# Kernel tuning notes

Measured on AMD Instinct MI355X. Metric: run time of the kernel, lower is better.

## Reference

```python
import jax, jax.numpy as jnp
import numpy as np

DIM = 256      # z feature dim
HEADS = 8
C = 64         # per-head dim == x channel dim
INNER = HEADS * C  # 512


def setup_inputs() -> dict:
    key = jax.random.key(0)
    ks = jax.random.split(key, 8)
    b, h, w, m = 8, 64, 64, 256
    x = jax.random.normal(ks[0], (b, C, h, w), dtype=jnp.float32)
    z = jax.random.normal(ks[1], (b, m, DIM), dtype=jnp.float32)
    s = 1.0 / np.sqrt(DIM)
    Wk = jax.random.normal(ks[2], (DIM, INNER), dtype=jnp.float32) * s
    bk = jnp.zeros((INNER,), dtype=jnp.float32)
    Wv = jax.random.normal(ks[3], (DIM, INNER), dtype=jnp.float32) * s
    bv = jnp.zeros((INNER,), dtype=jnp.float32)
    Wo = jax.random.normal(ks[4], (INNER, C), dtype=jnp.float32) * (1.0 / np.sqrt(INNER))
    bo = jnp.zeros((C,), dtype=jnp.float32)
    return {"x": x, "z": z, "Wk": Wk, "bk": bk, "Wv": Wv, "bv": bv, "Wo": Wo, "bo": bo}


def reference(x, z, Wk, bk, Wv, bv, Wo, bo):
    b, c, h, w = x.shape
    m = z.shape[1]
    heads = Wk.shape[1] // c
    hw = h * w
    # Faithful to torch: raw view (b,c,h,w)->(b,hw,c), then repeat along feature
    # dim and raw view into (b, heads, hw, c).
    q = jnp.tile(x.reshape(b, hw, c), (1, 1, heads)).reshape(b, heads, hw, c)
    # k/v: Linear then raw view (b, m, heads*c) -> (b, heads, m, c).
    k = (z @ Wk + bk).reshape(b, heads, m, c)
    v = (z @ Wv + bv).reshape(b, heads, m, c)
    scale = c ** (-0.5)
    dots = jnp.einsum('bhlc,bhmc->bhlm', q, k) * scale
    attn = jax.nn.softmax(dots, axis=-1)
    out = jnp.einsum('bhlm,bhmc->bhlc', attn, v)
    out = jnp.transpose(out, (0, 2, 1, 3)).reshape(b, hw, heads * c)  # b l (h c)
    out = out @ Wo + bo  # (b, hw, c)
    # Faithful raw view back to (b, c, h, w), then residual.
    return x + out.reshape(b, c, h, w)
```

## Files before the change

### kernel.cpp

```cpp
#include <hip/hip_runtime.h>

#define HEADS 8
#define CH    64
#define HW    4096
#define MTOK  256
#define DIMZ  256
#define INNER 512
#define LROWS 512

typedef __attribute__((ext_vector_type(8))) __bf16 bf16x8;
typedef __attribute__((ext_vector_type(4))) float  f32x4;

__device__ __forceinline__ unsigned f2bf(float f) {
  unsigned u = __float_as_uint(f);
  return (u + 0x7fffu + ((u >> 16) & 1u)) >> 16;
}

__device__ __forceinline__ bf16x8 ld_bf8(const unsigned short* p) {
  uint4 v = *(const uint4*)p;
  return __builtin_bit_cast(bf16x8, v);
}

__global__ __launch_bounds__(256) void prep(
    const float* __restrict__ z, const float* __restrict__ Wk,
    const float* __restrict__ Wv, const float* __restrict__ Wo,
    unsigned short* __restrict__ zbf, unsigned short* __restrict__ WkT,
    unsigned short* __restrict__ WvT, unsigned short* __restrict__ WoT) {
  const int blk = blockIdx.x, tid = threadIdx.x;
  if (blk < 512) {
    int i = (blk * 256 + tid) * 4;
    float4 f = *(const float4*)(z + i);
    uint2 w;
    w.x = f2bf(f.x) | (f2bf(f.y) << 16);
    w.y = f2bf(f.z) | (f2bf(f.w) << 16);
    *(uint2*)(zbf + i) = w;
  } else if (blk < 768) {
    const bool isK = blk < 640;
    const float* __restrict__ W = isK ? Wk : Wv;
    unsigned short* __restrict__ WT = isK ? WkT : WvT;
    int gidx = (blk - (isK ? 512 : 640)) * 256 + tid;
    int n = gidx >> 6, k0 = (gidx & 63) * 4;
    uint2 w;
    w.x = f2bf(W[(size_t)k0 * INNER + n])       | (f2bf(W[(size_t)(k0 + 1) * INNER + n]) << 16);
    w.y = f2bf(W[(size_t)(k0 + 2) * INNER + n]) | (f2bf(W[(size_t)(k0 + 3) * INNER + n]) << 16);
    *(uint2*)(WT + (size_t)n * DIMZ + k0) = w;
  } else {
    int gidx = (blk - 768) * 256 + tid;
    int n = gidx >> 7, k0 = (gidx & 127) * 4;
    uint2 w;
    w.x = f2bf(Wo[(size_t)k0 * CH + n])       | (f2bf(Wo[(size_t)(k0 + 1) * CH + n]) << 16);
    w.y = f2bf(Wo[(size_t)(k0 + 2) * CH + n]) | (f2bf(Wo[(size_t)(k0 + 3) * CH + n]) << 16);
    *(uint2*)(WoT + (size_t)n * INNER + k0) = w;
  }
}

__global__ __launch_bounds__(256) void kv_mfma(
    const unsigned short* __restrict__ zbf,
    const unsigned short* __restrict__ WkT, const float* __restrict__ bk,
    const unsigned short* __restrict__ WvT, const float* __restrict__ bv,
    unsigned short* __restrict__ klin, unsigned short* __restrict__ vt) {
  const int t = threadIdx.x;
  const int lane = t & 63, wid = t >> 6;
  const int c = lane & 15, g = lane >> 4;
  const int mb = blockIdx.x;
  const int bn = blockIdx.y;
  const bool isK = bn < 8;
  const int nb = bn & 7;
  const unsigned short* __restrict__ WT = isK ? WkT : WvT;
  const float* __restrict__ bias = isK ? bk : bv;
  const int m0 = mb * 64 + (wid >> 1) * 32;
  const int n0 = nb * 64 + (wid & 1) * 32;

  f32x4 acc[2][2];
#pragma unroll
  for (int i = 0; i < 2; ++i)
#pragma unroll
    for (int j = 0; j < 2; ++j) acc[i][j] = (f32x4)0.f;

#pragma unroll
  for (int s = 0; s < 8; ++s) {
    const int k0 = s * 32;
    bf16x8 a0 = ld_bf8(zbf + (size_t)(m0 + c) * DIMZ + k0 + 8 * g);
    bf16x8 a1 = ld_bf8(zbf + (size_t)(m0 + 16 + c) * DIMZ + k0 + 8 * g);
    bf16x8 b0 = ld_bf8(WT + (size_t)(n0 + c) * DIMZ + k0 + 8 * g);
    bf16x8 b1 = ld_bf8(WT + (size_t)(n0 + 16 + c) * DIMZ + k0 + 8 * g);
    if (isK) {
      acc[0][0] = __builtin_amdgcn_mfma_f32_16x16x32_bf16(b0, a0, acc[0][0], 0, 0, 0);
      acc[0][1] = __builtin_amdgcn_mfma_f32_16x16x32_bf16(b1, a0, acc[0][1], 0, 0, 0);
      acc[1][0] = __builtin_amdgcn_mfma_f32_16x16x32_bf16(b0, a1, acc[1][0], 0, 0, 0);
      acc[1][1] = __builtin_amdgcn_mfma_f32_16x16x32_bf16(b1, a1, acc[1][1], 0, 0, 0);
    } else {
      acc[0][0] = __builtin_amdgcn_mfma_f32_16x16x32_bf16(a0, b0, acc[0][0], 0, 0, 0);
      acc[0][1] = __builtin_amdgcn_mfma_f32_16x16x32_bf16(a0, b1, acc[0][1], 0, 0, 0);
      acc[1][0] = __builtin_amdgcn_mfma_f32_16x16x32_bf16(a1, b0, acc[1][0], 0, 0, 0);
      acc[1][1] = __builtin_amdgcn_mfma_f32_16x16x32_bf16(a1, b1, acc[1][1], 0, 0, 0);
    }
  }

  if (isK) {
#pragma unroll
    for (int mt = 0; mt < 2; ++mt)
#pragma unroll
      for (int nt = 0; nt < 2; ++nt) {
        const int m = m0 + mt * 16 + c;
        const int n = n0 + nt * 16 + 4 * g;
        float4 b4 = *(const float4*)(bias + n);
        uint2 w;
        w.x = f2bf(acc[mt][nt][0] + b4.x) | (f2bf(acc[mt][nt][1] + b4.y) << 16);
        w.y = f2bf(acc[mt][nt][2] + b4.z) | (f2bf(acc[mt][nt][3] + b4.w) << 16);
        *(uint2*)(klin + (size_t)m * INNER + n) = w;
      }
  } else {
#pragma unroll
    for (int mt = 0; mt < 2; ++mt)
#pragma unroll
      for (int nt = 0; nt < 2; ++nt) {
        const int n = n0 + nt * 16 + c;
        const float bn1 = bias[n];
        const int m = m0 + mt * 16 + 4 * g;
        const int bb = m >> 8;
        const int mtk = m & 255;
        const int h = mtk >> 5, t0 = mtk & 31;
        const int cc = n & 63, cb = n >> 6;
        uint2 w;
        w.x = f2bf(acc[mt][nt][0] + bn1) | (f2bf(acc[mt][nt][1] + bn1) << 16);
        w.y = f2bf(acc[mt][nt][2] + bn1) | (f2bf(acc[mt][nt][3] + bn1) << 16);
        *(uint2*)(vt + ((size_t)((bb * HEADS + h) * CH + cc)) * MTOK + cb * 32 + t0) = w;
      }
  }
}

__global__ __launch_bounds__(64) void attn_mfma(
    const float* __restrict__ x,
    const unsigned short* __restrict__ kbf,
    const unsigned short* __restrict__ vtbf,
    unsigned short* __restrict__ out2) {
  __shared__ unsigned short Psh[16 * 256];
  char* Pb = (char*)Psh;
  const int t = threadIdx.x;
  const int c = t & 15, g = t >> 4;
  const int bid = blockIdx.x;
  const int lt = bid & 31, hh = (bid >> 5) & 7, b = bid >> 8;
  const int qbase = lt * 16;
  const float* xs = x + (size_t)b * (HW * CH) + (size_t)hh * (LROWS * CH);
  const unsigned short* Kg = kbf + ((size_t)b * MTOK + hh * 32) * INNER;
  const unsigned short* Vg = vtbf + (size_t)(b * HEADS + hh) * (CH * MTOK);

  const float qs = 0.125f * 1.44269504089f;
  bf16x8 qfr[2];
#pragma unroll
  for (int ks = 0; ks < 2; ++ks) {
    const float* qp = xs + (size_t)(qbase + c) * CH + 32 * ks + 8 * g;
    float4 f0 = *(const float4*)qp;
    float4 f1 = *(const float4*)(qp + 4);
    uint4 u;
    u.x = f2bf(f0.x * qs) | (f2bf(f0.y * qs) << 16);
    u.y = f2bf(f0.z * qs) | (f2bf(f0.w * qs) << 16);
    u.z = f2bf(f1.x * qs) | (f2bf(f1.y * qs) << 16);
    u.w = f2bf(f1.z * qs) | (f2bf(f1.w * qs) << 16);
    qfr[ks] = __builtin_bit_cast(bf16x8, u);
  }

  f32x4 acc[16];
#pragma unroll
  for (int kf = 0; kf < 16; ++kf) acc[kf] = (f32x4)0.f;
#pragma unroll
  for (int kf = 0; kf < 16; ++kf) {
    const unsigned short* kp =
        Kg + (size_t)((kf & 1) * 16 + c) * INNER + (kf >> 1) * 64 + 8 * g;
    bf16x8 a0 = ld_bf8(kp);
    bf16x8 a1 = ld_bf8(kp + 32);
    acc[kf] = __builtin_amdgcn_mfma_f32_16x16x32_bf16(a0, qfr[0], acc[kf], 0, 0, 0);
    acc[kf] = __builtin_amdgcn_mfma_f32_16x16x32_bf16(a1, qfr[1], acc[kf], 0, 0, 0);
  }

  float m = acc[0][0];
#pragma unroll
  for (int kf = 0; kf < 16; ++kf)
    m = fmaxf(m, fmaxf(fmaxf(acc[kf][0], acc[kf][1]),
                       fmaxf(acc[kf][2], acc[kf][3])));
  m = fmaxf(m, __shfl_xor(m, 16));
  m = fmaxf(m, __shfl_xor(m, 32));
  float sum = 0.f;
  const int rowb = c * 512;
#pragma unroll
  for (int kf = 0; kf < 16; ++kf) {
    float e0 = exp2f(acc[kf][0] - m);
    float e1 = exp2f(acc[kf][1] - m);
    float e2 = exp2f(acc[kf][2] - m);
    float e3 = exp2f(acc[kf][3] - m);
    sum += (e0 + e1) + (e2 + e3);
    uint2 w;
    w.x = f2bf(e0) | (f2bf(e1) << 16);
    w.y = f2bf(e2) | (f2bf(e3) << 16);
    int off = (rowb + (16 * kf + 4 * g) * 2) ^ ((c & 7) << 4);
    *(uint2*)(Pb + off) = w;
  }
  sum += __shfl_xor(sum, 16);
  sum += __shfl_xor(sum, 32);
  const float inv = 1.f / sum;
  asm volatile("" ::: "memory");

  f32x4 o[4];
#pragma unroll
  for (int cf = 0; cf < 4; ++cf) o[cf] = (f32x4)0.f;
#pragma unroll
  for (int ks = 0; ks < 8; ++ks) {
    bf16x8 p = __builtin_bit_cast(bf16x8,
        *(const uint4*)(Pb + ((c * 512 + (32 * ks + 8 * g) * 2) ^ ((c & 7) << 4))));
#pragma unroll
    for (int cf = 0; cf < 4; ++cf) {
      bf16x8 a = ld_bf8(Vg + (size_t)(16 * cf + c) * MTOK + 32 * ks + 8 * g);
      o[cf] = __builtin_amdgcn_mfma_f32_16x16x32_bf16(a, p, o[cf], 0, 0, 0);
    }
  }

#pragma unroll
  for (int cf = 0; cf < 4; ++cf) {
    f32x4 r = o[cf] * inv;
    size_t row = (size_t)b * LROWS + qbase + c;
    uint2 w;
    w.x = f2bf(r[0]) | (f2bf(r[1]) << 16);
    w.y = f2bf(r[2]) | (f2bf(r[3]) << 16);
    *(uint2*)(out2 + row * INNER + hh * CH + 16 * cf + 4 * g) = w;
  }
}

__global__ __launch_bounds__(256) void proj_mfma(
    const unsigned short* __restrict__ out2,
    const unsigned short* __restrict__ WoT, const float* __restrict__ bo,
    const float* __restrict__ x, float* __restrict__ y) {
  __shared__ __align__(16) float Sp[4][16][68];
  const int t = threadIdx.x, lane = t & 63, wid = t >> 6;
  const int c = lane & 15, g = lane >> 4;
  const int m0 = blockIdx.x * 16;
  const int kw = wid * 128;

  f32x4 acc[4];
#pragma unroll
  for (int nt = 0; nt < 4; ++nt) acc[nt] = (f32x4)0.f;
#pragma unroll
  for (int s = 0; s < 4; ++s) {
    const int k0 = kw + s * 32;
    bf16x8 bfr = ld_bf8(out2 + (size_t)(m0 + c) * INNER + k0 + 8 * g);
#pragma unroll
    for (int nt = 0; nt < 4; ++nt) {
      bf16x8 afr = ld_bf8(WoT + (size_t)(nt * 16 + c) * INNER + k0 + 8 * g);
      acc[nt] = __builtin_amdgcn_mfma_f32_16x16x32_bf16(afr, bfr, acc[nt], 0, 0, 0);
    }
  }
#pragma unroll
  for (int nt = 0; nt < 4; ++nt)
    *(f32x4*)&Sp[wid][c][nt * 16 + 4 * g] = acc[nt];
  __syncthreads();

  const int i = t >> 4, j0 = (t & 15) * 4;
  float4 s0 = *(const float4*)&Sp[0][i][j0];
  float4 s1 = *(const float4*)&Sp[1][i][j0];
  float4 s2 = *(const float4*)&Sp[2][i][j0];
  float4 s3 = *(const float4*)&Sp[3][i][j0];
  float4 b4 = *(const float4*)(bo + j0);
  float4 o4 = make_float4(s0.x + s1.x + s2.x + s3.x + b4.x,
                          s0.y + s1.y + s2.y + s3.y + b4.y,
                          s0.z + s1.z + s2.z + s3.z + b4.z,
                          s0.w + s1.w + s2.w + s3.w + b4.w);
  const int m = m0 + i, bb = m >> 9, L = m & 511;
  const float* xr = x + (size_t)bb * (HW * CH) + (size_t)L * 8 * CH + j0;
  float*       yr = y + (size_t)bb * (HW * CH) + (size_t)L * 8 * CH + j0;
#pragma unroll
  for (int r = 0; r < 8; ++r) {
    float4 xv = *(const float4*)(xr + r * CH);
    float4 ov = make_float4(o4.x + xv.x, o4.y + xv.y, o4.z + xv.z, o4.w + xv.w);
    *(float4*)(yr + r * CH) = ov;
  }
}

extern "C" void kernel_launch(void* const* d_in, const int* in_sizes, int n_in,
                              void* d_out, int out_size, void* d_ws, size_t ws_size,
                              hipStream_t stream) {
  const float* x  = (const float*)d_in[0];
  const float* z  = (const float*)d_in[1];
  const float* Wk = (const float*)d_in[2];
  const float* bk = (const float*)d_in[3];
  const float* Wv = (const float*)d_in[4];
  const float* bv = (const float*)d_in[5];
  const float* Wo = (const float*)d_in[6];
  const float* bo = (const float*)d_in[7];
  float* y = (float*)d_out;

  unsigned short* zbf  = (unsigned short*)d_ws;
  unsigned short* WkT  = zbf  + (size_t)2048 * DIMZ;
  unsigned short* WvT  = WkT  + (size_t)INNER * DIMZ;
  unsigned short* WoT  = WvT  + (size_t)INNER * DIMZ;
  unsigned short* klin = WoT  + (size_t)CH * INNER;
  unsigned short* vt   = klin + (size_t)2048 * INNER;
  unsigned short* out2 = vt   + (size_t)2048 * INNER;

  prep<<<800, 256, 0, stream>>>(z, Wk, Wv, Wo, zbf, WkT, WvT, WoT);
  dim3 gA(32, 16);
  kv_mfma<<<gA, 256, 0, stream>>>(zbf, WkT, bk, WvT, bv, klin, vt);
  attn_mfma<<<2048, 64, 0, stream>>>(x, klin, vt, out2);
  proj_mfma<<<256, 256, 0, stream>>>(out2, WoT, bo, x, y);
}
```

Baseline: 47.73 us.

## Fuse K/V projection into attention kernel with LDS-resident K and V

Merges the z conversion, K/V linear projection and attention into one kernel. Each 512-thread block computes the 32-token K and V slice it needs straight from fp32 z into shared memory, then eight waves run attention over 128 query rows. This removes the global round trip of the klin and vt intermediates, the separate z conversion and two kernel launches. In exchange, each of the four query-chunk blocks per (batch, head) recomputes the same K/V projection, and the 128 KB shared-memory footprint allows only one block per CU.

Measured after the change: 45.95 us. 1.04x faster.

```diff
diff --git a/kernel.cpp b/kernel.cpp
--- a/kernel.cpp
+++ b/kernel.cpp
@@ -21,31 +21,35 @@
   return __builtin_bit_cast(bf16x8, v);
 }
 
-__global__ __launch_bounds__(256) void prep(
-    const float* __restrict__ z, const float* __restrict__ Wk,
-    const float* __restrict__ Wv, const float* __restrict__ Wo,
-    unsigned short* __restrict__ zbf, unsigned short* __restrict__ WkT,
-    unsigned short* __restrict__ WvT, unsigned short* __restrict__ WoT) {
+__device__ __forceinline__ bf16x8 cvt8(const float* p) {
+  float4 f0 = *(const float4*)p;
+  float4 f1 = *(const float4*)(p + 4);
+  uint4 u;
+  u.x = f2bf(f0.x) | (f2bf(f0.y) << 16);
+  u.y = f2bf(f0.z) | (f2bf(f0.w) << 16);
+  u.z = f2bf(f1.x) | (f2bf(f1.y) << 16);
+  u.w = f2bf(f1.z) | (f2bf(f1.w) << 16);
+  return __builtin_bit_cast(bf16x8, u);
+}
+
+__global__ __launch_bounds__(256) void prep_w(
+    const float* __restrict__ Wk, const float* __restrict__ Wv,
+    const float* __restrict__ Wo,
+    unsigned short* __restrict__ WkT, unsigned short* __restrict__ WvT,
+    unsigned short* __restrict__ WoT) {
   const int blk = blockIdx.x, tid = threadIdx.x;
-  if (blk < 512) {
-    int i = (blk * 256 + tid) * 4;
-    float4 f = *(const float4*)(z + i);
-    uint2 w;
-    w.x = f2bf(f.x) | (f2bf(f.y) << 16);
-    w.y = f2bf(f.z) | (f2bf(f.w) << 16);
-    *(uint2*)(zbf + i) = w;
-  } else if (blk < 768) {
-    const bool isK = blk < 640;
+  if (blk < 256) {
+    const bool isK = blk < 128;
     const float* __restrict__ W = isK ? Wk : Wv;
     unsigned short* __restrict__ WT = isK ? WkT : WvT;
-    int gidx = (blk - (isK ? 512 : 640)) * 256 + tid;
+    int gidx = (blk & 127) * 256 + tid;
     int n = gidx >> 6, k0 = (gidx & 63) * 4;
     uint2 w;
     w.x = f2bf(W[(size_t)k0 * INNER + n])       | (f2bf(W[(size_t)(k0 + 1) * INNER + n]) << 16);
     w.y = f2bf(W[(size_t)(k0 + 2) * INNER + n]) | (f2bf(W[(size_t)(k0 + 3) * INNER + n]) << 16);
     *(uint2*)(WT + (size_t)n * DIMZ + k0) = w;
   } else {
-    int gidx = (blk - 768) * 256 + tid;
+    int gidx = (blk - 256) * 256 + tid;
     int n = gidx >> 7, k0 = (gidx & 127) * 4;
     uint2 w;
     w.x = f2bf(Wo[(size_t)k0 * CH + n])       | (f2bf(Wo[(size_t)(k0 + 1) * CH + n]) << 16);
@@ -54,97 +58,100 @@
   }
 }
 
-__global__ __launch_bounds__(256) void kv_mfma(
-    const unsigned short* __restrict__ zbf,
+__global__ __launch_bounds__(512) void fused_attn(
+    const float* __restrict__ x, const float* __restrict__ z,
     const unsigned short* __restrict__ WkT, const float* __restrict__ bk,
     const unsigned short* __restrict__ WvT, const float* __restrict__ bv,
-    unsigned short* __restrict__ klin, unsigned short* __restrict__ vt) {
+    unsigned short* __restrict__ out2) {
+  __shared__ __align__(16) char lds[131072];
   const int t = threadIdx.x;
   const int lane = t & 63, wid = t >> 6;
   const int c = lane & 15, g = lane >> 4;
-  const int mb = blockIdx.x;
-  const int bn = blockIdx.y;
-  const bool isK = bn < 8;
-  const int nb = bn & 7;
-  const unsigned short* __restrict__ WT = isK ? WkT : WvT;
-  const float* __restrict__ bias = isK ? bk : bv;
-  const int m0 = mb * 64 + (wid >> 1) * 32;
-  const int n0 = nb * 64 + (wid & 1) * 32;
-
-  f32x4 acc[2][2];
-#pragma unroll
-  for (int i = 0; i < 2; ++i)
-#pragma unroll
-    for (int j = 0; j < 2; ++j) acc[i][j] = (f32x4)0.f;
-
-#pragma unroll
-  for (int s = 0; s < 8; ++s) {
-    const int k0 = s * 32;
-    bf16x8 a0 = ld_bf8(zbf + (size_t)(m0 + c) * DIMZ + k0 + 8 * g);
-    bf16x8 a1 = ld_bf8(zbf + (size_t)(m0 + 16 + c) * DIMZ + k0 + 8 * g);
-    bf16x8 b0 = ld_bf8(WT + (size_t)(n0 + c) * DIMZ + k0 + 8 * g);
-    bf16x8 b1 = ld_bf8(WT + (size_t)(n0 + 16 + c) * DIMZ + k0 + 8 * g);
+  const int bid = blockIdx.x;
+  const int qc = bid & 3, hh = (bid >> 2) & 7, b = bid >> 5;
+
+  {
+    const bool isK = wid < 4;
+    const unsigned short* __restrict__ WT = isK ? WkT : WvT;
+    const float* __restrict__ bias = isK ? bk : bv;
+    const float* zs = z + ((size_t)b * MTOK + hh * 32) * DIMZ;
+
+    f32x4 acc[4][2][2];
+#pragma unroll
+    for (int tt = 0; tt < 4; ++tt)
+#pragma unroll
+      for (int i = 0; i < 2; ++i)
+#pragma unroll
+        for (int j = 0; j < 2; ++j) acc[tt][i][j] = (f32x4)0.f;
+
+#pragma unroll
+    for (int s = 0; s < 8; ++s) {
+      const int k0 = s * 32;
+      bf16x8 a0 = cvt8(zs + (size_t)c * DIMZ + k0 + 8 * g);
+      bf16x8 a1 = cvt8(zs + (size_t)(16 + c) * DIMZ + k0 + 8 * g);
+#pragma unroll
+      for (int tt = 0; tt < 4; ++tt) {
+        const int n0 = ((wid & 3) * 4 + tt) * 32;
+        bf16x8 b0 = ld_bf8(WT + (size_t)(n0 + c) * DIMZ + k0 + 8 * g);
+        bf16x8 b1 = ld_bf8(WT + (size_t)(n0 + 16 + c) * DIMZ + k0 + 8 * g);
+        if (isK) {
+          acc[tt][0][0] = __builtin_amdgcn_mfma_f32_16x16x32_bf16(b0, a0, acc[tt][0][0], 0, 0, 0);
+          acc[tt][0][1] = __builtin_amdgcn_mfma_f32_16x16x32_bf16(b1, a0, acc[tt][0][1], 0, 0, 0);
+          acc[tt][1][0] = __builtin_amdgcn_mfma_f32_16x16x32_bf16(b0, a1, acc[tt][1][0], 0, 0, 0);
+          acc[tt][1][1] = __builtin_amdgcn_mfma_f32_16x16x32_bf16(b1, a1, acc[tt][1][1], 0, 0, 0);
+        } else {
+          acc[tt][0][0] = __builtin_amdgcn_mfma_f32_16x16x32_bf16(a0, b0, acc[tt][0][0], 0, 0, 0);
+          acc[tt][0][1] = __builtin_amdgcn_mfma_f32_16x16x32_bf16(a0, b1, acc[tt][0][1], 0, 0, 0);
+          acc[tt][1][0] = __builtin_amdgcn_mfma_f32_16x16x32_bf16(a1, b0, acc[tt][1][0], 0, 0, 0);
+          acc[tt][1][1] = __builtin_amdgcn_mfma_f32_16x16x32_bf16(a1, b1, acc[tt][1][1], 0, 0, 0);
+        }
+      }
+    }
     if (isK) {
-      acc[0][0] = __builtin_amdgcn_mfma_f32_16x16x32_bf16(b0, a0, acc[0][0], 0, 0, 0);
-      acc[0][1] = __builtin_amdgcn_mfma_f32_16x16x32_bf16(b1, a0, acc[0][1], 0, 0, 0);
-      acc[1][0] = __builtin_amdgcn_mfma_f32_16x16x32_bf16(b0, a1, acc[1][0], 0, 0, 0);
-      acc[1][1] = __builtin_amdgcn_mfma_f32_16x16x32_bf16(b1, a1, acc[1][1], 0, 0, 0);
+#pragma unroll
+      for (int tt = 0; tt < 4; ++tt) {
+        const int n0 = ((wid & 3) * 4 + tt) * 32;
+#pragma unroll
+        for (int mt = 0; mt < 2; ++mt)
+#pragma unroll
+          for (int nt = 0; nt < 2; ++nt) {
+            const int nb4 = n0 + nt * 16 + 4 * g;
+            float4 b4 = *(const float4*)(bias + nb4);
+            const int key = (nb4 >> 6) * 32 + mt * 16 + c;
+            const int ch0 = nb4 & 63;
+            uint2 w;
+            w.x = f2bf(acc[tt][mt][nt][0] + b4.x) | (f2bf(acc[tt][mt][nt][1] + b4.y) << 16);
+            w.y = f2bf(acc[tt][mt][nt][2] + b4.z) | (f2bf(acc[tt][mt][nt][3] + b4.w) << 16);
+            *(uint2*)(lds + ((key * 128 + ch0 * 2) ^ ((key & 7) << 4))) = w;
+          }
+      }
     } else {
-      acc[0][0] = __builtin_amdgcn_mfma_f32_16x16x32_bf16(a0, b0, acc[0][0], 0, 0, 0);
-      acc[0][1] = __builtin_amdgcn_mfma_f32_16x16x32_bf16(a0, b1, acc[0][1], 0, 0, 0);
-      acc[1][0] = __builtin_amdgcn_mfma_f32_16x16x32_bf16(a1, b0, acc[1][0], 0, 0, 0);
-      acc[1][1] = __builtin_amdgcn_mfma_f32_16x16x32_bf16(a1, b1, acc[1][1], 0, 0, 0);
+#pragma unroll
+      for (int tt = 0; tt < 4; ++tt) {
+        const int n0 = ((wid & 3) * 4 + tt) * 32;
+#pragma unroll
+        for (int mt = 0; mt < 2; ++mt)
+#pragma unroll
+          for (int nt = 0; nt < 2; ++nt) {
+            const int n = n0 + nt * 16 + c;
+            const float bn1 = bias[n];
+            const int ch = n & 63;
+            const int key0 = (n >> 6) * 32 + mt * 16 + 4 * g;
+            uint2 w;
+            w.x = f2bf(acc[tt][mt][nt][0] + bn1) | (f2bf(acc[tt][mt][nt][1] + bn1) << 16);
+            w.y = f2bf(acc[tt][mt][nt][2] + bn1) | (f2bf(acc[tt][mt][nt][3] + bn1) << 16);
+            *(uint2*)(lds + 32768 + ((ch * 512 + key0 * 2) ^ ((ch & 7) << 4))) = w;
+          }
+      }
     }
   }
-
-  if (isK) {
-#pragma unroll
-    for (int mt = 0; mt < 2; ++mt)
-#pragma unroll
-      for (int nt = 0; nt < 2; ++nt) {
-        const int m = m0 + mt * 16 + c;
-        const int n = n0 + nt * 16 + 4 * g;
-        float4 b4 = *(const float4*)(bias + n);
-        uint2 w;
-        w.x = f2bf(acc[mt][nt][0] + b4.x) | (f2bf(acc[mt][nt][1] + b4.y) << 16);
-        w.y = f2bf(acc[mt][nt][2] + b4.z) | (f2bf(acc[mt][nt][3] + b4.w) << 16);
-        *(uint2*)(klin + (size_t)m * INNER + n) = w;
-      }
-  } else {
-#pragma unroll
-    for (int mt = 0; mt < 2; ++mt)
-#pragma unroll
-      for (int nt = 0; nt < 2; ++nt) {
-        const int n = n0 + nt * 16 + c;
-        const float bn1 = bias[n];
-        const int m = m0 + mt * 16 + 4 * g;
-        const int bb = m >> 8;
-        const int mtk = m & 255;
-        const int h = mtk >> 5, t0 = mtk & 31;
-        const int cc = n & 63, cb = n >> 6;
-        uint2 w;
-        w.x = f2bf(acc[mt][nt][0] + bn1) | (f2bf(acc[mt][nt][1] + bn1) << 16);
-        w.y = f2bf(acc[mt][nt][2] + bn1) | (f2bf(acc[mt][nt][3] + bn1) << 16);
-        *(uint2*)(vt + ((size_t)((bb * HEADS + h) * CH + cc)) * MTOK + cb * 32 + t0) = w;
-      }
-  }
-}
-
-__global__ __launch_bounds__(64) void attn_mfma(
-    const float* __restrict__ x,
-    const unsigned short* __restrict__ kbf,
-    const unsigned short* __restrict__ vtbf,
-    unsigned short* __restrict__ out2) {
-  __shared__ unsigned short Psh[16 * 256];
-  char* Pb = (char*)Psh;
-  const int t = threadIdx.x;
-  const int c = t & 15, g = t >> 4;
-  const int bid = blockIdx.x;
-  const int lt = bid & 31, hh = (bid >> 5) & 7, b = bid >> 8;
-  const int qbase = lt * 16;
+  __syncthreads();
+
+  const char* Kb = lds;
+  const char* Vb = lds + 32768;
+  char* Pb = lds + 65536 + wid * 8192;
+  const int qbase = qc * 128 + wid * 16;
   const float* xs = x + (size_t)b * (HW * CH) + (size_t)hh * (LROWS * CH);
-  const unsigned short* Kg = kbf + ((size_t)b * MTOK + hh * 32) * INNER;
-  const unsigned short* Vg = vtbf + (size_t)(b * HEADS + hh) * (CH * MTOK);
 
   const float qs = 0.125f * 1.44269504089f;
   bf16x8 qfr[2];
@@ -166,10 +173,11 @@
   for (int kf = 0; kf < 16; ++kf) acc[kf] = (f32x4)0.f;
 #pragma unroll
   for (int kf = 0; kf < 16; ++kf) {
-    const unsigned short* kp =
-        Kg + (size_t)((kf & 1) * 16 + c) * INNER + (kf >> 1) * 64 + 8 * g;
-    bf16x8 a0 = ld_bf8(kp);
-    bf16x8 a1 = ld_bf8(kp + 32);
+    const int key = 16 * kf + c;
+    bf16x8 a0 = __builtin_bit_cast(bf16x8,
+        *(const uint4*)(Kb + ((key * 128 + 16 * g) ^ ((key & 7) << 4))));
+    bf16x8 a1 = __builtin_bit_cast(bf16x8,
+        *(const uint4*)(Kb + ((key * 128 + 64 + 16 * g) ^ ((key & 7) << 4))));
     acc[kf] = __builtin_amdgcn_mfma_f32_16x16x32_bf16(a0, qfr[0], acc[kf], 0, 0, 0);
     acc[kf] = __builtin_amdgcn_mfma_f32_16x16x32_bf16(a1, qfr[1], acc[kf], 0, 0, 0);
   }
@@ -193,8 +201,7 @@
     uint2 w;
     w.x = f2bf(e0) | (f2bf(e1) << 16);
     w.y = f2bf(e2) | (f2bf(e3) << 16);
-    int off = (rowb + (16 * kf + 4 * g) * 2) ^ ((c & 7) << 4);
-    *(uint2*)(Pb + off) = w;
+    *(uint2*)(Pb + ((rowb + (16 * kf + 4 * g) * 2) ^ ((c & 7) << 4))) = w;
   }
   sum += __shfl_xor(sum, 16);
   sum += __shfl_xor(sum, 32);
@@ -210,7 +217,9 @@
         *(const uint4*)(Pb + ((c * 512 + (32 * ks + 8 * g) * 2) ^ ((c & 7) << 4))));
 #pragma unroll
     for (int cf = 0; cf < 4; ++cf) {
-      bf16x8 a = ld_bf8(Vg + (size_t)(16 * cf + c) * MTOK + 32 * ks + 8 * g);
+      const int ch = 16 * cf + c;
+      bf16x8 a = __builtin_bit_cast(bf16x8,
+          *(const uint4*)(Vb + ((ch * 512 + (32 * ks + 8 * g) * 2) ^ ((ch & 7) << 4))));
       o[cf] = __builtin_amdgcn_mfma_f32_16x16x32_bf16(a, p, o[cf], 0, 0, 0);
     }
   }
@@ -288,17 +297,12 @@
   const float* bo = (const float*)d_in[7];
   float* y = (float*)d_out;
 
-  unsigned short* zbf  = (unsigned short*)d_ws;
-  unsigned short* WkT  = zbf  + (size_t)2048 * DIMZ;
-  unsigned short* WvT  = WkT  + (size_t)INNER * DIMZ;
-  unsigned short* WoT  = WvT  + (size_t)INNER * DIMZ;
-  unsigned short* klin = WoT  + (size_t)CH * INNER;
-  unsigned short* vt   = klin + (size_t)2048 * INNER;
-  unsigned short* out2 = vt   + (size_t)2048 * INNER;
-
-  prep<<<800, 256, 0, stream>>>(z, Wk, Wv, Wo, zbf, WkT, WvT, WoT);
-  dim3 gA(32, 16);
-  kv_mfma<<<gA, 256, 0, stream>>>(zbf, WkT, bk, WvT, bv, klin, vt);
-  attn_mfma<<<2048, 64, 0, stream>>>(x, klin, vt, out2);
+  unsigned short* WkT  = (unsigned short*)d_ws;
+  unsigned short* WvT  = WkT + (size_t)INNER * DIMZ;
+  unsigned short* WoT  = WvT + (size_t)INNER * DIMZ;
+  unsigned short* out2 = WoT + (size_t)CH * INNER;
+
+  prep_w<<<288, 256, 0, stream>>>(Wk, Wv, Wo, WkT, WvT, WoT);
+  fused_attn<<<256, 512, 0, stream>>>(x, z, WkT, bk, WvT, bv, out2);
   proj_mfma<<<256, 256, 0, stream>>>(out2, WoT, bo, x, y);
 }
```

## Fuse prep into KV projection and attention with output projection

Applied to the files above, without the earlier changes.

Removes the separate prep kernel by having the K/V projection read fp32 z and weights directly, converting and transposing the weight tiles through shared memory, with an extra row of blocks transposing Wo. Attention and the output projection are merged into one 512-thread block per batch and 16-query chunk: eight waves each compute one head, write bf16 outputs to LDS, then split-K project and reduce before the residual add. This drops two launches and the out2 global round trip. In exchange, attention parallelism falls from 2048 to 256 blocks with heavy LDS use, and z is converted redundantly across column blocks.

Measured after the change: 46.41 us. 1.03x faster.

```diff
diff --git a/kernel.cpp b/kernel.cpp
--- a/kernel.cpp
+++ b/kernel.cpp
@@ -21,55 +21,59 @@
   return __builtin_bit_cast(bf16x8, v);
 }
 
-__global__ __launch_bounds__(256) void prep(
-    const float* __restrict__ z, const float* __restrict__ Wk,
-    const float* __restrict__ Wv, const float* __restrict__ Wo,
-    unsigned short* __restrict__ zbf, unsigned short* __restrict__ WkT,
-    unsigned short* __restrict__ WvT, unsigned short* __restrict__ WoT) {
-  const int blk = blockIdx.x, tid = threadIdx.x;
-  if (blk < 512) {
-    int i = (blk * 256 + tid) * 4;
-    float4 f = *(const float4*)(z + i);
-    uint2 w;
-    w.x = f2bf(f.x) | (f2bf(f.y) << 16);
-    w.y = f2bf(f.z) | (f2bf(f.w) << 16);
-    *(uint2*)(zbf + i) = w;
-  } else if (blk < 768) {
-    const bool isK = blk < 640;
-    const float* __restrict__ W = isK ? Wk : Wv;
-    unsigned short* __restrict__ WT = isK ? WkT : WvT;
-    int gidx = (blk - (isK ? 512 : 640)) * 256 + tid;
-    int n = gidx >> 6, k0 = (gidx & 63) * 4;
-    uint2 w;
-    w.x = f2bf(W[(size_t)k0 * INNER + n])       | (f2bf(W[(size_t)(k0 + 1) * INNER + n]) << 16);
-    w.y = f2bf(W[(size_t)(k0 + 2) * INNER + n]) | (f2bf(W[(size_t)(k0 + 3) * INNER + n]) << 16);
-    *(uint2*)(WT + (size_t)n * DIMZ + k0) = w;
-  } else {
-    int gidx = (blk - 768) * 256 + tid;
-    int n = gidx >> 7, k0 = (gidx & 127) * 4;
-    uint2 w;
-    w.x = f2bf(Wo[(size_t)k0 * CH + n])       | (f2bf(Wo[(size_t)(k0 + 1) * CH + n]) << 16);
-    w.y = f2bf(Wo[(size_t)(k0 + 2) * CH + n]) | (f2bf(Wo[(size_t)(k0 + 3) * CH + n]) << 16);
-    *(uint2*)(WoT + (size_t)n * INNER + k0) = w;
-  }
-}
-
-__global__ __launch_bounds__(256) void kv_mfma(
-    const unsigned short* __restrict__ zbf,
-    const unsigned short* __restrict__ WkT, const float* __restrict__ bk,
-    const unsigned short* __restrict__ WvT, const float* __restrict__ bv,
-    unsigned short* __restrict__ klin, unsigned short* __restrict__ vt) {
+__device__ __forceinline__ bf16x8 cvt8(const float* p) {
+  float4 f0 = *(const float4*)p;
+  float4 f1 = *(const float4*)(p + 4);
+  uint4 u;
+  u.x = f2bf(f0.x) | (f2bf(f0.y) << 16);
+  u.y = f2bf(f0.z) | (f2bf(f0.w) << 16);
+  u.z = f2bf(f1.x) | (f2bf(f1.y) << 16);
+  u.w = f2bf(f1.z) | (f2bf(f1.w) << 16);
+  return __builtin_bit_cast(bf16x8, u);
+}
+
+__global__ __launch_bounds__(256) void kv_gen(
+    const float* __restrict__ z,
+    const float* __restrict__ Wk, const float* __restrict__ bk,
+    const float* __restrict__ Wv, const float* __restrict__ bv,
+    const float* __restrict__ Wo,
+    unsigned short* __restrict__ klin, unsigned short* __restrict__ vt,
+    unsigned short* __restrict__ WoT) {
+  __shared__ unsigned short Tw[64][40];
+  __shared__ float Tf[64][65];
   const int t = threadIdx.x;
+  const int bn = blockIdx.y;
+
+  if (bn == 16) {
+    if (blockIdx.x >= 8) return;
+    const int k0 = blockIdx.x * 64;
+    const int rr = t >> 6, cc = t & 63;
+#pragma unroll
+    for (int it = 0; it < 16; ++it) {
+      int r = it * 4 + rr;
+      Tf[r][cc] = Wo[(size_t)(k0 + r) * CH + cc];
+    }
+    __syncthreads();
+    const int nr = t >> 5, kp = t & 31;
+#pragma unroll
+    for (int it = 0; it < 8; ++it) {
+      int n = it * 8 + nr;
+      unsigned w = f2bf(Tf[kp * 2][n]) | (f2bf(Tf[kp * 2 + 1][n]) << 16);
+      *(unsigned*)(WoT + (size_t)n * INNER + k0 + kp * 2) = w;
+    }
+    return;
+  }
+
   const int lane = t & 63, wid = t >> 6;
   const int c = lane & 15, g = lane >> 4;
   const int mb = blockIdx.x;
-  const int bn = blockIdx.y;
   const bool isK = bn < 8;
   const int nb = bn & 7;
-  const unsigned short* __restrict__ WT = isK ? WkT : WvT;
+  const float* __restrict__ W    = isK ? Wk : Wv;
   const float* __restrict__ bias = isK ? bk : bv;
   const int m0 = mb * 64 + (wid >> 1) * 32;
   const int n0 = nb * 64 + (wid & 1) * 32;
+  const int nloc = (wid & 1) * 32;
 
   f32x4 acc[2][2];
 #pragma unroll
@@ -77,13 +81,27 @@
 #pragma unroll
     for (int j = 0; j < 2; ++j) acc[i][j] = (f32x4)0.f;
 
-#pragma unroll
   for (int s = 0; s < 8; ++s) {
     const int k0 = s * 32;
-    bf16x8 a0 = ld_bf8(zbf + (size_t)(m0 + c) * DIMZ + k0 + 8 * g);
-    bf16x8 a1 = ld_bf8(zbf + (size_t)(m0 + 16 + c) * DIMZ + k0 + 8 * g);
-    bf16x8 b0 = ld_bf8(WT + (size_t)(n0 + c) * DIMZ + k0 + 8 * g);
-    bf16x8 b1 = ld_bf8(WT + (size_t)(n0 + 16 + c) * DIMZ + k0 + 8 * g);
+    {
+      const int kk = t >> 3, nn = (t & 7) * 8;
+      const float* wp = W + (size_t)(k0 + kk) * INNER + nb * 64 + nn;
+      float4 w0 = *(const float4*)wp;
+      float4 w1 = *(const float4*)(wp + 4);
+      Tw[nn + 0][kk] = (unsigned short)f2bf(w0.x);
+      Tw[nn + 1][kk] = (unsigned short)f2bf(w0.y);
+      Tw[nn + 2][kk] = (unsigned short)f2bf(w0.z);
+      Tw[nn + 3][kk] = (unsigned short)f2bf(w0.w);
+      Tw[nn + 4][kk] = (unsigned short)f2bf(w1.x);
+      Tw[nn + 5][kk] = (unsigned short)f2bf(w1.y);
+      Tw[nn + 6][kk] = (unsigned short)f2bf(w1.z);
+      Tw[nn + 7][kk] = (unsigned short)f2bf(w1.w);
+    }
+    __syncthreads();
+    bf16x8 a0 = cvt8(z + (size_t)(m0 + c) * DIMZ + k0 + 8 * g);
+    bf16x8 a1 = cvt8(z + (size_t)(m0 + 16 + c) * DIMZ + k0 + 8 * g);
+    bf16x8 b0 = *(const bf16x8*)&Tw[nloc + c][8 * g];
+    bf16x8 b1 = *(const bf16x8*)&Tw[nloc + 16 + c][8 * g];
     if (isK) {
       acc[0][0] = __builtin_amdgcn_mfma_f32_16x16x32_bf16(b0, a0, acc[0][0], 0, 0, 0);
       acc[0][1] = __builtin_amdgcn_mfma_f32_16x16x32_bf16(b1, a0, acc[0][1], 0, 0, 0);
@@ -95,6 +113,7 @@
       acc[1][0] = __builtin_amdgcn_mfma_f32_16x16x32_bf16(a1, b0, acc[1][0], 0, 0, 0);
       acc[1][1] = __builtin_amdgcn_mfma_f32_16x16x32_bf16(a1, b1, acc[1][1], 0, 0, 0);
     }
+    __syncthreads();
   }
 
   if (isK) {
@@ -121,157 +140,158 @@
         const int bb = m >> 8;
         const int mtk = m & 255;
         const int h = mtk >> 5, t0 = mtk & 31;
-        const int cc = n & 63, cb = n >> 6;
+        const int cc2 = n & 63, cb = n >> 6;
         uint2 w;
         w.x = f2bf(acc[mt][nt][0] + bn1) | (f2bf(acc[mt][nt][1] + bn1) << 16);
         w.y = f2bf(acc[mt][nt][2] + bn1) | (f2bf(acc[mt][nt][3] + bn1) << 16);
-        *(uint2*)(vt + ((size_t)((bb * HEADS + h) * CH + cc)) * MTOK + cb * 32 + t0) = w;
+        *(uint2*)(vt + ((size_t)((bb * HEADS + h) * CH + cc2)) * MTOK + cb * 32 + t0) = w;
       }
   }
 }
 
-__global__ __launch_bounds__(64) void attn_mfma(
+__global__ __launch_bounds__(512) void attnproj(
     const float* __restrict__ x,
     const unsigned short* __restrict__ kbf,
     const unsigned short* __restrict__ vtbf,
-    unsigned short* __restrict__ out2) {
-  __shared__ unsigned short Psh[16 * 256];
-  char* Pb = (char*)Psh;
+    const unsigned short* __restrict__ WoT, const float* __restrict__ bo,
+    float* __restrict__ y) {
+  __shared__ __align__(16) char lds[65536 + 16384 + 8 * 16 * 68 * 4];
+  char* Osh = lds + 65536;
+  float* Sp = (float*)(lds + 65536 + 16384);
   const int t = threadIdx.x;
-  const int c = t & 15, g = t >> 4;
+  const int lane = t & 63, wid = t >> 6;
+  const int c = lane & 15, g = lane >> 4;
   const int bid = blockIdx.x;
-  const int lt = bid & 31, hh = (bid >> 5) & 7, b = bid >> 8;
-  const int qbase = lt * 16;
-  const float* xs = x + (size_t)b * (HW * CH) + (size_t)hh * (LROWS * CH);
-  const unsigned short* Kg = kbf + ((size_t)b * MTOK + hh * 32) * INNER;
-  const unsigned short* Vg = vtbf + (size_t)(b * HEADS + hh) * (CH * MTOK);
-
-  const float qs = 0.125f * 1.44269504089f;
-  bf16x8 qfr[2];
-#pragma unroll
-  for (int ks = 0; ks < 2; ++ks) {
-    const float* qp = xs + (size_t)(qbase + c) * CH + 32 * ks + 8 * g;
-    float4 f0 = *(const float4*)qp;
-    float4 f1 = *(const float4*)(qp + 4);
-    uint4 u;
-    u.x = f2bf(f0.x * qs) | (f2bf(f0.y * qs) << 16);
-    u.y = f2bf(f0.z * qs) | (f2bf(f0.w * qs) << 16);
-    u.z = f2bf(f1.x * qs) | (f2bf(f1.y * qs) << 16);
-    u.w = f2bf(f1.z * qs) | (f2bf(f1.w * qs) << 16);
-    qfr[ks] = __builtin_bit_cast(bf16x8, u);
-  }
-
-  f32x4 acc[16];
-#pragma unroll
-  for (int kf = 0; kf < 16; ++kf) acc[kf] = (f32x4)0.f;
-#pragma unroll
-  for (int kf = 0; kf < 16; ++kf) {
-    const unsigned short* kp =
-        Kg + (size_t)((kf & 1) * 16 + c) * INNER + (kf >> 1) * 64 + 8 * g;
-    bf16x8 a0 = ld_bf8(kp);
-    bf16x8 a1 = ld_bf8(kp + 32);
-    acc[kf] = __builtin_amdgcn_mfma_f32_16x16x32_bf16(a0, qfr[0], acc[kf], 0, 0, 0);
-    acc[kf] = __builtin_amdgcn_mfma_f32_16x16x32_bf16(a1, qfr[1], acc[kf], 0, 0, 0);
-  }
-
-  float m = acc[0][0];
-#pragma unroll
-  for (int kf = 0; kf < 16; ++kf)
-    m = fmaxf(m, fmaxf(fmaxf(acc[kf][0], acc[kf][1]),
-                       fmaxf(acc[kf][2], acc[kf][3])));
-  m = fmaxf(m, __shfl_xor(m, 16));
-  m = fmaxf(m, __shfl_xor(m, 32));
-  float sum = 0.f;
-  const int rowb = c * 512;
-#pragma unroll
-  for (int kf = 0; kf < 16; ++kf) {
-    float e0 = exp2f(acc[kf][0] - m);
-    float e1 = exp2f(acc[kf][1] - m);
-    float e2 = exp2f(acc[kf][2] - m);
-    float e3 = exp2f(acc[kf][3] - m);
-    sum += (e0 + e1) + (e2 + e3);
-    uint2 w;
-    w.x = f2bf(e0) | (f2bf(e1) << 16);
-    w.y = f2bf(e2) | (f2bf(e3) << 16);
-    int off = (rowb + (16 * kf + 4 * g) * 2) ^ ((c & 7) << 4);
-    *(uint2*)(Pb + off) = w;
-  }
-  sum += __shfl_xor(sum, 16);
-  sum += __shfl_xor(sum, 32);
-  const float inv = 1.f / sum;
-  asm volatile("" ::: "memory");
-
-  f32x4 o[4];
-#pragma unroll
-  for (int cf = 0; cf < 4; ++cf) o[cf] = (f32x4)0.f;
-#pragma unroll
-  for (int ks = 0; ks < 8; ++ks) {
-    bf16x8 p = __builtin_bit_cast(bf16x8,
-        *(const uint4*)(Pb + ((c * 512 + (32 * ks + 8 * g) * 2) ^ ((c & 7) << 4))));
+  const int qc = bid & 31, b = bid >> 5;
+  const int hh = wid;
+  const int qbase = qc * 16;
+  char* Pb = lds + wid * 8192;
+
+  {
+    const float* xs = x + (size_t)b * (HW * CH) + (size_t)hh * (LROWS * CH);
+    const unsigned short* Kg = kbf + ((size_t)b * MTOK + hh * 32) * INNER;
+    const unsigned short* Vg = vtbf + (size_t)(b * HEADS + hh) * (CH * MTOK);
+
+    const float qs = 0.125f * 1.44269504089f;
+    bf16x8 qfr[2];
+#pragma unroll
+    for (int ks = 0; ks < 2; ++ks) {
+      const float* qp = xs + (size_t)(qbase + c) * CH + 32 * ks + 8 * g;
+      float4 f0 = *(const float4*)qp;
+      float4 f1 = *(const float4*)(qp + 4);
+      uint4 u;
+      u.x = f2bf(f0.x * qs) | (f2bf(f0.y * qs) << 16);
+      u.y = f2bf(f0.z * qs) | (f2bf(f0.w * qs) << 16);
+      u.z = f2bf(f1.x * qs) | (f2bf(f1.y * qs) << 16);
+      u.w = f2bf(f1.z * qs) | (f2bf(f1.w * qs) << 16);
+      qfr[ks] = __builtin_bit_cast(bf16x8, u);
+    }
+
+    f32x4 acc[16];
+#pragma unroll
+    for (int kf = 0; kf < 16; ++kf) acc[kf] = (f32x4)0.f;
+#pragma unroll
+    for (int kf = 0; kf < 16; ++kf) {
+      const unsigned short* kp =
+          Kg + (size_t)((kf & 1) * 16 + c) * INNER + (kf >> 1) * 64 + 8 * g;
+      bf16x8 a0 = ld_bf8(kp);
+      bf16x8 a1 = ld_bf8(kp + 32);
+      acc[kf] = __builtin_amdgcn_mfma_f32_16x16x32_bf16(a0, qfr[0], acc[kf], 0, 0, 0);
+      acc[kf] = __builtin_amdgcn_mfma_f32_16x16x32_bf16(a1, qfr[1], acc[kf], 0, 0, 0);
+    }
+
+    float m = acc[0][0];
+#pragma unroll
+    for (int kf = 0; kf < 16; ++kf)
+      m = fmaxf(m, fmaxf(fmaxf(acc[kf][0], acc[kf][1]),
+                         fmaxf(acc[kf][2], acc[kf][3])));
+    m = fmaxf(m, __shfl_xor(m, 16));
+    m = fmaxf(m, __shfl_xor(m, 32));
+    float sum = 0.f;
+    const int rowb = c * 512;
+#pragma unroll
+    for (int kf = 0; kf < 16; ++kf) {
+      float e0 = exp2f(acc[kf][0] - m);
+      float e1 = exp2f(acc[kf][1] - m);
+      float e2 = exp2f(acc[kf][2] - m);
+      float e3 = exp2f(acc[kf][3] - m);
+      sum += (e0 + e1) + (e2 + e3);
+      uint2 w;
+      w.x = f2bf(e0) | (f2bf(e1) << 16);
+      w.y = f2bf(e2) | (f2bf(e3) << 16);
+      *(uint2*)(Pb + ((rowb + (16 * kf + 4 * g) * 2) ^ ((c & 7) << 4))) = w;
+    }
+    sum += __shfl_xor(sum, 16);
+    sum += __shfl_xor(sum, 32);
+    const float inv = 1.f / sum;
+    asm volatile("" ::: "memory");
+
+    f32x4 o[4];
+#pragma unroll
+    for (int cf = 0; cf < 4; ++cf) o[cf] = (f32x4)0.f;
+#pragma unroll
+    for (int ks = 0; ks < 8; ++ks) {
+      bf16x8 p = __builtin_bit_cast(bf16x8,
+          *(const uint4*)(Pb + ((c * 512 + (32 * ks + 8 * g) * 2) ^ ((c & 7) << 4))));
+#pragma unroll
+      for (int cf = 0; cf < 4; ++cf) {
+        bf16x8 a = ld_bf8(Vg + (size_t)(16 * cf + c) * MTOK + 32 * ks + 8 * g);
+        o[cf] = __builtin_amdgcn_mfma_f32_16x16x32_bf16(a, p, o[cf], 0, 0, 0);
+      }
+    }
+
 #pragma unroll
     for (int cf = 0; cf < 4; ++cf) {
-      bf16x8 a = ld_bf8(Vg + (size_t)(16 * cf + c) * MTOK + 32 * ks + 8 * g);
-      o[cf] = __builtin_amdgcn_mfma_f32_16x16x32_bf16(a, p, o[cf], 0, 0, 0);
-    }
-  }
-
-#pragma unroll
-  for (int cf = 0; cf < 4; ++cf) {
-    f32x4 r = o[cf] * inv;
-    size_t row = (size_t)b * LROWS + qbase + c;
-    uint2 w;
-    w.x = f2bf(r[0]) | (f2bf(r[1]) << 16);
-    w.y = f2bf(r[2]) | (f2bf(r[3]) << 16);
-    *(uint2*)(out2 + row * INNER + hh * CH + 16 * cf + 4 * g) = w;
-  }
-}
-
-__global__ __launch_bounds__(256) void proj_mfma(
-    const unsigned short* __restrict__ out2,
-    const unsigned short* __restrict__ WoT, const float* __restrict__ bo,
-    const float* __restrict__ x, float* __restrict__ y) {
-  __shared__ __align__(16) float Sp[4][16][68];
-  const int t = threadIdx.x, lane = t & 63, wid = t >> 6;
-  const int c = lane & 15, g = lane >> 4;
-  const int m0 = blockIdx.x * 16;
-  const int kw = wid * 128;
-
-  f32x4 acc[4];
-#pragma unroll
-  for (int nt = 0; nt < 4; ++nt) acc[nt] = (f32x4)0.f;
-#pragma unroll
-  for (int s = 0; s < 4; ++s) {
-    const int k0 = kw + s * 32;
-    bf16x8 bfr = ld_bf8(out2 + (size_t)(m0 + c) * INNER + k0 + 8 * g);
-#pragma unroll
-    for (int nt = 0; nt < 4; ++nt) {
-      bf16x8 afr = ld_bf8(WoT + (size_t)(nt * 16 + c) * INNER + k0 + 8 * g);
-      acc[nt] = __builtin_amdgcn_mfma_f32_16x16x32_bf16(afr, bfr, acc[nt], 0, 0, 0);
-    }
-  }
-#pragma unroll
-  for (int nt = 0; nt < 4; ++nt)
-    *(f32x4*)&Sp[wid][c][nt * 16 + 4 * g] = acc[nt];
+      f32x4 r = o[cf] * inv;
+      uint2 w;
+      w.x = f2bf(r[0]) | (f2bf(r[1]) << 16);
+      w.y = f2bf(r[2]) | (f2bf(r[3]) << 16);
+      int off = (c * 1024 + (hh * 64 + 16 * cf + 4 * g) * 2) ^ ((c & 7) << 4);
+      *(uint2*)(Osh + off) = w;
+    }
+  }
   __syncthreads();
 
-  const int i = t >> 4, j0 = (t & 15) * 4;
-  float4 s0 = *(const float4*)&Sp[0][i][j0];
-  float4 s1 = *(const float4*)&Sp[1][i][j0];
-  float4 s2 = *(const float4*)&Sp[2][i][j0];
-  float4 s3 = *(const float4*)&Sp[3][i][j0];
+  {
+    const int kw = wid * 64;
+    f32x4 acc[4];
+#pragma unroll
+    for (int nt = 0; nt < 4; ++nt) acc[nt] = (f32x4)0.f;
+#pragma unroll
+    for (int s = 0; s < 2; ++s) {
+      const int k0 = kw + s * 32;
+      bf16x8 bfr = __builtin_bit_cast(bf16x8,
+          *(const uint4*)(Osh + ((c * 1024 + (k0 + 8 * g) * 2) ^ ((c & 7) << 4))));
+#pragma unroll
+      for (int nt = 0; nt < 4; ++nt) {
+        bf16x8 afr = ld_bf8(WoT + (size_t)(nt * 16 + c) * INNER + k0 + 8 * g);
+        acc[nt] = __builtin_amdgcn_mfma_f32_16x16x32_bf16(afr, bfr, acc[nt], 0, 0, 0);
+      }
+    }
+#pragma unroll
+    for (int nt = 0; nt < 4; ++nt)
+      *(f32x4*)&Sp[(wid * 16 + c) * 68 + nt * 16 + 4 * g] = acc[nt];
+  }
+  __syncthreads();
+
+  const int i = t >> 5, jj = t & 31;
+  const int j0 = (jj & 15) * 4, rh = jj >> 4;
   float4 b4 = *(const float4*)(bo + j0);
-  float4 o4 = make_float4(s0.x + s1.x + s2.x + s3.x + b4.x,
-                          s0.y + s1.y + s2.y + s3.y + b4.y,
-                          s0.z + s1.z + s2.z + s3.z + b4.z,
-                          s0.w + s1.w + s2.w + s3.w + b4.w);
-  const int m = m0 + i, bb = m >> 9, L = m & 511;
-  const float* xr = x + (size_t)bb * (HW * CH) + (size_t)L * 8 * CH + j0;
-  float*       yr = y + (size_t)bb * (HW * CH) + (size_t)L * 8 * CH + j0;
-#pragma unroll
-  for (int r = 0; r < 8; ++r) {
-    float4 xv = *(const float4*)(xr + r * CH);
+  float4 o4 = b4;
+#pragma unroll
+  for (int w = 0; w < 8; ++w) {
+    float4 s = *(const float4*)&Sp[(w * 16 + i) * 68 + j0];
+    o4.x += s.x; o4.y += s.y; o4.z += s.z; o4.w += s.w;
+  }
+  const int L = qbase + i;
+  const float* xr = x + (size_t)b * (HW * CH) + (size_t)L * 8 * CH + j0;
+  float*       yr = y + (size_t)b * (HW * CH) + (size_t)L * 8 * CH + j0;
+#pragma unroll
+  for (int r = 0; r < 4; ++r) {
+    const int rr = rh * 4 + r;
+    float4 xv = *(const float4*)(xr + rr * CH);
     float4 ov = make_float4(o4.x + xv.x, o4.y + xv.y, o4.z + xv.z, o4.w + xv.w);
-    *(float4*)(yr + r * CH) = ov;
+    *(float4*)(yr + rr * CH) = ov;
   }
 }
 
@@ -288,17 +308,10 @@
   const float* bo = (const float*)d_in[7];
   float* y = (float*)d_out;
 
-  unsigned short* zbf  = (unsigned short*)d_ws;
-  unsigned short* WkT  = zbf  + (size_t)2048 * DIMZ;
-  unsigned short* WvT  = WkT  + (size_t)INNER * DIMZ;
-  unsigned short* WoT  = WvT  + (size_t)INNER * DIMZ;
-  unsigned short* klin = WoT  + (size_t)CH * INNER;
+  unsigned short* klin = (unsigned short*)d_ws;
   unsigned short* vt   = klin + (size_t)2048 * INNER;
-  unsigned short* out2 = vt   + (size_t)2048 * INNER;
-
-  prep<<<800, 256, 0, stream>>>(z, Wk, Wv, Wo, zbf, WkT, WvT, WoT);
-  dim3 gA(32, 16);
-  kv_mfma<<<gA, 256, 0, stream>>>(zbf, WkT, bk, WvT, bv, klin, vt);
-  attn_mfma<<<2048, 64, 0, stream>>>(x, klin, vt, out2);
-  proj_mfma<<<256, 256, 0, stream>>>(out2, WoT, bo, x, y);
-}
+  unsigned short* WoT  = vt   + (size_t)2048 * INNER;
+
+  kv_gen<<<dim3(32, 17), 256, 0, stream>>>(z, Wk, bk, Wv, bv, Wo, klin, vt, WoT);
+  attnproj<<<256, 512, 0, stream>>>(x, klin, vt, WoT, bo, y);
+}
```
